# Kernel optimization log

Measured on AMD Instinct MI355X. Metric: run time of the kernel, lower is better.

## Reference

```python
import jax, jax.numpy as jnp
import numpy as np

N, B, E, H, L, NF = 32768, 2048, 524288, 128, 7, 10
NODE_F = 60  # 10 frames * (loc 3 + vel 3)
OUT_F = 30   # 10 frames * 3


def _mlp(x, W1, b1, W2, b2):
    return jax.nn.relu(x @ W1 + b1) @ W2 + b2


def _lin(key, fan_in, fan_out):
    s = 1.0 / np.sqrt(fan_in)
    kw, kb = jax.random.split(key)
    W = jax.random.uniform(kw, (fan_in, fan_out), jnp.float32, -s, s)
    b = jax.random.uniform(kb, (fan_out,), jnp.float32, -s, s)
    return W, b


def setup_inputs() -> dict:
    key = jax.random.key(0)
    ks = jax.random.split(key, 12)
    p = {}
    p["loc"] = jax.random.normal(ks[0], (N, NF, 3), jnp.float32)
    p["vel"] = jax.random.normal(ks[1], (N, NF, 3), jnp.float32)
    p["y"] = jax.random.normal(ks[2], (N, NF, 3), jnp.float32)
    p["edge_index"] = jax.random.randint(ks[3], (2, E), 0, N, dtype=jnp.int64)
    p["batch_size"] = B
    # embedder: Linear(60,H) -> ReLU -> Linear(H,H)
    p["emb_W1"], p["emb_b1"] = _lin(ks[4], NODE_F, H)
    p["emb_W2"], p["emb_b2"] = _lin(ks[5], H, H)
    # per-layer message net Linear(2H,H)->ReLU->Linear(H,H); update net Linear(2H,H)->ReLU->Linear(H,H)
    mW1, mb1, mW2, mb2, uW1, ub1, uW2, ub2 = [], [], [], [], [], [], [], []
    for i in range(L):
        k = jax.random.fold_in(ks[6], i)
        k1, k2, k3, k4 = jax.random.split(k, 4)
        a, b = _lin(k1, 2 * H, H); mW1.append(a); mb1.append(b)
        a, b = _lin(k2, H, H); mW2.append(a); mb2.append(b)
        a, b = _lin(k3, 2 * H, H); uW1.append(a); ub1.append(b)
        a, b = _lin(k4, H, H); uW2.append(a); ub2.append(b)
    p["msg_W1"] = jnp.stack(mW1); p["msg_b1"] = jnp.stack(mb1)
    p["msg_W2"] = jnp.stack(mW2); p["msg_b2"] = jnp.stack(mb2)
    p["upd_W1"] = jnp.stack(uW1); p["upd_b1"] = jnp.stack(ub1)
    p["upd_W2"] = jnp.stack(uW2); p["upd_b2"] = jnp.stack(ub2)
    # head: Linear(H,H) -> ReLU -> Linear(H,30)
    p["head_W1"], p["head_b1"] = _lin(ks[7], H, H)
    p["head_W2"], p["head_b2"] = _lin(ks[8], H, OUT_F)
    return p


def reference(loc, vel, y, edge_index, batch_size,
              emb_W1, emb_b1, emb_W2, emb_b2,
              msg_W1, msg_b1, msg_W2, msg_b2,
              upd_W1, upd_b1, upd_W2, upd_b2,
              head_W1, head_b1, head_W2, head_b2):
    n = loc.shape[0]
    src, dst = edge_index[0], edge_index[1]  # x_j = x[src], x_i = x[dst] (PyG source_to_target)
    x = jnp.concatenate([loc, vel], axis=-1).reshape(n, -1)  # (N, 60)
    x = _mlp(x, emb_W1, emb_b1, emb_W2, emb_b2)              # (N, H)
    for i in range(L):
        m_in = jnp.concatenate([x[dst], x[src]], axis=-1)    # (E, 2H) cat(x_i, x_j)
        msg = _mlp(m_in, msg_W1[i], msg_b1[i], msg_W2[i], msg_b2[i])  # (E, H)
        agg = jax.ops.segment_sum(msg, dst, num_segments=n)  # scatter-add at targets
        x = _mlp(jnp.concatenate([x, agg], axis=-1), upd_W1[i], upd_b1[i], upd_W2[i], upd_b2[i])
    x = _mlp(x, head_W1, head_b1, head_W2, head_b2)          # (N, 30)
    loc_pred = x.reshape(n, NF, 3) + loc
    d = jnp.sqrt(jnp.sum((loc_pred - y) ** 2, axis=-1))      # (N, NF)
    ade_loss = d.reshape(batch_size, -1, NF).mean(axis=-1).mean(axis=-1)  # (B,)
    fde = jnp.sqrt(jnp.sum((loc_pred[:, -1, :] - y[:, -1, :]) ** 2, axis=-1))  # (N,)
    fde_loss = fde.reshape(batch_size, -1).mean(axis=-1)     # (B,)
    backprop_loss = ade_loss.mean()
    return backprop_loss, ade_loss, fde_loss
```

## Files before the change

### kernel.cpp

```cpp
#include <hip/hip_runtime.h>
#include <hip/hip_bf16.h>
#include <stdint.h>

#define HH 128

typedef __attribute__((ext_vector_type(8))) short short8;
typedef __attribute__((ext_vector_type(4))) float floatx4;

typedef __attribute__((address_space(3))) uint32_t lds_u32_t;
typedef const __attribute__((address_space(1))) uint32_t gbl_u32_t;

__device__ __forceinline__ void gl_lds16(const void* g, void* l) {
  __builtin_amdgcn_global_load_lds((gbl_u32_t*)g, (lds_u32_t*)l, 16, 0, 0);
}

__device__ __forceinline__ float bf2f(short v) {
  union { uint32_t u; float f; } x; x.u = ((uint32_t)(uint16_t)v) << 16; return x.f;
}
__device__ __forceinline__ short f2bf(float f) {
  union { float f; uint32_t u; } x; x.f = f;
  uint32_t r = x.u + 0x7fffu + ((x.u >> 16) & 1u);
  return (short)(r >> 16);
}
__device__ __forceinline__ float rdf(const void* p, int i, int fl) {
  return fl ? bf2f(((const short*)p)[i]) : ((const float*)p)[i];
}


__global__ void detect_zero(const int* __restrict__ eidx, int* iflag, int* dflag,
                            int* __restrict__ counts, float* accp, int* ticket,
                            const uint32_t* __restrict__ loc, int N) {
  int g = blockIdx.x * 256 + threadIdx.x;
  if (g < N) counts[g] = 0;
  if (blockIdx.x == 0) {
    __shared__ int nz, cnt;
    if (threadIdx.x == 0) { nz = 0; cnt = 0; *accp = 0.f; *ticket = 0; }
    __syncthreads();
    int any = 0;
    for (int i = threadIdx.x; i < 1024; i += 256) any |= (eidx[2 * i + 1] != 0);
    if (any) atomicOr(&nz, 1);
    uint32_t u = loc[threadIdx.x];
    int e = (u >> 7) & 0xFF;
    if (e >= 100 && e <= 140) atomicAdd(&cnt, 1);
    __syncthreads();
    if (threadIdx.x == 0) {
      *iflag = (nz == 0) ? 1 : 0;
      *dflag = (cnt >= 192) ? 1 : 0;
    }
  }
}


__global__ void pad_input(const void* __restrict__ loc, const void* __restrict__ vel,
                          short* __restrict__ dst, const int* __restrict__ dflag) {
  int fl = *dflag;
  int idx = blockIdx.x * 256 + threadIdx.x;
  int j = idx & 63, i = idx >> 6;
  short v = 0;
  if (j < 60) {
    int f = j / 6, c = j % 6;
    float x = (c < 3) ? rdf(loc, (i * 10 + f) * 3 + c, fl)
                      : rdf(vel, (i * 10 + f) * 3 + (c - 3), fl);
    v = f2bf(x);
  }
  dst[idx] = v;
}

struct WPrep {
  const void* src[8];
  unsigned long long dstoff[8];
  int L[8], K[8], Nn[8], Kp[8], Np[8];
  int bstart[9];
};

__global__ void prep_w(WPrep a, short* __restrict__ wbase, const int* __restrict__ dflag) {
  int fl = *dflag;
  int b = blockIdx.x;
  int s = 0;
  while (b >= a.bstart[s + 1]) ++s;
  int idx = (b - a.bstart[s]) * 256 + threadIdx.x;
  int Kp = a.Kp[s], Np = a.Np[s], K = a.K[s], Nn = a.Nn[s];
  int tot = a.L[s] * Np * Kp;
  if (idx >= tot) return;
  int k = idx % Kp; int rest = idx / Kp; int n = rest % Np; int l = rest / Np;
  short v = 0;
  if (k < K && n < Nn) v = f2bf(rdf(a.src[s], (l * K + k) * Nn + n, fl));
  wbase[a.dstoff[s] + idx] = v;
}

struct BPrep {
  const void* src[8];
  int n[8];
  int estart[9];
};

__global__ void prep_b(BPrep a, float* __restrict__ bias, const int* __restrict__ dflag) {
  int fl = *dflag;
  int idx = blockIdx.x * 256 + threadIdx.x;
  if (idx >= a.estart[8]) return;
  int s = 0;
  while (idx >= a.estart[s + 1]) ++s;
  int j = idx - a.estart[s];
  bias[idx] = (j < a.n[s]) ? rdf(a.src[s], j, fl) : 0.0f;
}


__global__ void fold_kernel(const short* __restrict__ updW1T, const short* __restrict__ msgW2T,
                            short* __restrict__ updW1Tf, const float* __restrict__ msgB2f,
                            float* __restrict__ b2U) {
  if (blockIdx.x < 896) {
    int idx = blockIdx.x * 256 + threadIdx.x;
    int k = idx & 255; int n = (idx >> 8) & 127; int l = idx >> 15;
    if (k < 128) { updW1Tf[idx] = updW1T[idx]; return; }
    int kk = k - 128;
    const short* w2 = msgW2T + l * 128 * 128;
    const short* u1 = updW1T + l * 128 * 256 + n * 256 + 128;
    float s = 0.f;
    for (int j = 0; j < 128; ++j) s += bf2f(w2[j * 128 + kk]) * bf2f(u1[j]);
    updW1Tf[idx] = f2bf(s);
  } else {
    int idx = (blockIdx.x - 896) * 256 + threadIdx.x;
    if (idx >= 7 * 128) return;
    int n = idx & 127, l = idx >> 7;
    const short* u1 = updW1T + l * 128 * 256 + n * 256 + 128;
    const float* b2 = msgB2f + l * 128;
    float s = 0.f;
    for (int j = 0; j < 128; ++j) s += b2[j] * bf2f(u1[j]);
    b2U[idx] = s;
  }
}


__global__ void hist_kernel(const int* __restrict__ eidx, const int* __restrict__ iflag,
                            int* __restrict__ counts, int E) {
  int e = blockIdx.x * 256 + threadIdx.x;
  if (e >= E) return;
  int fl = *iflag;
  int d = fl ? eidx[2 * (E + e)] : eidx[E + e];
  atomicAdd(&counts[d], 1);
}

__global__ void scan_bsum(const int* __restrict__ counts, int* __restrict__ bsums, int N) {
  int i = blockIdx.x * 256 + threadIdx.x;
  int v = (i < N) ? counts[i] : 0;
#pragma unroll
  for (int off = 1; off < 64; off <<= 1) v += __shfl_xor(v, off);
  __shared__ int ws4[4];
  if ((threadIdx.x & 63) == 0) ws4[threadIdx.x >> 6] = v;
  __syncthreads();
  if (threadIdx.x == 0) bsums[blockIdx.x] = ws4[0] + ws4[1] + ws4[2] + ws4[3];
}

__global__ void scan_final(const int* __restrict__ counts, const int* __restrict__ bsums,
                           int* __restrict__ row_start, int* __restrict__ cursor,
                           float* __restrict__ deg, int N, int E) {
  int t = threadIdx.x;
  __shared__ int shb[2];
  __shared__ int wsum[4];
  int v = (t < 128 && t < (int)blockIdx.x) ? bsums[t] : 0;
#pragma unroll
  for (int off = 1; off < 64; off <<= 1) v += __shfl_xor(v, off);
  if (t == 0) shb[0] = v;
  if (t == 64) shb[1] = v;
  int i = blockIdx.x * 256 + t;
  int c = (i < N) ? counts[i] : 0;
  int lane = t & 63, w = t >> 6;
  int x = c;
#pragma unroll
  for (int off = 1; off < 64; off <<= 1) {
    int u = __shfl_up(x, off);
    if (lane >= off) x += u;
  }
  if (lane == 63) wsum[w] = x;
  __syncthreads();
  int wpre = 0;
#pragma unroll
  for (int k = 0; k < 4; ++k)
    if (k < w) wpre += wsum[k];
  int excl = shb[0] + shb[1] + wpre + x - c;
  if (i < N) {
    row_start[i] = excl;
    cursor[i] = excl;
    deg[i] = (float)c;
  }
  if (i == N - 1) row_start[N] = E;
}

__global__ void scatter_kernel(const int* __restrict__ eidx, const int* __restrict__ iflag,
                               int* __restrict__ cursor, int* __restrict__ ssrc, int E) {
  int e = blockIdx.x * 256 + threadIdx.x;
  if (e >= E) return;
  int fl = *iflag;
  int d = fl ? eidx[2 * (E + e)] : eidx[E + e];
  int sv = fl ? eidx[2 * e] : eidx[e];
  int pos = atomicAdd(&cursor[d], 1);
  ssrc[pos] = sv;
}


__global__ __launch_bounds__(256)
void edge_agg(const uint32_t* __restrict__ Pp, const uint32_t* __restrict__ Qp,
              const int* __restrict__ ssrc, const int* __restrict__ row_start,
              uint32_t* __restrict__ Hagg, int Ntot) {
  int w = threadIdx.x >> 6, lane = threadIdx.x & 63;
  int d = blockIdx.x * 4 + w;
  if (d >= Ntot) return;
  uint32_t pv = Pp[(size_t)d * 64 + lane];
  float px = bf2f((short)(pv & 0xffff));
  float py = bf2f((short)(pv >> 16));
  int s0 = row_start[d], s1 = row_start[d + 1];
  float ax = 0.f, ay = 0.f;
  int e = s0;
  for (; e + 8 <= s1; e += 8) {
    int idx[8]; uint32_t q[8];
#pragma unroll
    for (int u = 0; u < 8; ++u) idx[u] = ssrc[e + u];
#pragma unroll
    for (int u = 0; u < 8; ++u) q[u] = Qp[(size_t)idx[u] * 64 + lane];
#pragma unroll
    for (int u = 0; u < 8; ++u) {
      float hx = px + bf2f((short)(q[u] & 0xffff));
      float hy = py + bf2f((short)(q[u] >> 16));
      ax += hx > 0.f ? hx : 0.f;
      ay += hy > 0.f ? hy : 0.f;
    }
  }
  if (e + 4 <= s1) {
    int idx[4]; uint32_t q[4];
#pragma unroll
    for (int u = 0; u < 4; ++u) idx[u] = ssrc[e + u];
#pragma unroll
    for (int u = 0; u < 4; ++u) q[u] = Qp[(size_t)idx[u] * 64 + lane];
#pragma unroll
    for (int u = 0; u < 4; ++u) {
      float hx = px + bf2f((short)(q[u] & 0xffff));
      float hy = py + bf2f((short)(q[u] >> 16));
      ax += hx > 0.f ? hx : 0.f;
      ay += hy > 0.f ? hy : 0.f;
    }
    e += 4;
  }
  if (e + 2 <= s1) {
    int i0 = ssrc[e], i1 = ssrc[e + 1];
    uint32_t q0 = Qp[(size_t)i0 * 64 + lane];
    uint32_t q1 = Qp[(size_t)i1 * 64 + lane];
    float hx = px + bf2f((short)(q0 & 0xffff)), hy = py + bf2f((short)(q0 >> 16));
    ax += hx > 0.f ? hx : 0.f; ay += hy > 0.f ? hy : 0.f;
    hx = px + bf2f((short)(q1 & 0xffff)); hy = py + bf2f((short)(q1 >> 16));
    ax += hx > 0.f ? hx : 0.f; ay += hy > 0.f ? hy : 0.f;
    e += 2;
  }
  if (e < s1) {
    int i0 = ssrc[e];
    uint32_t q0 = Qp[(size_t)i0 * 64 + lane];
    float hx = px + bf2f((short)(q0 & 0xffff));
    float hy = py + bf2f((short)(q0 >> 16));
    ax += hx > 0.f ? hx : 0.f;
    ay += hy > 0.f ? hy : 0.f;
  }
  uint32_t packed = (uint32_t)(uint16_t)f2bf(ax) | ((uint32_t)(uint16_t)f2bf(ay) << 16);
  Hagg[(size_t)d * 64 + lane] = packed;
}


__device__ __forceinline__ void write_aslots64(char* lds, const floatx4 v[2][4],
                                               int wr, int wc, int quad, int l16) {
#pragma unroll
  for (int mt = 0; mt < 2; ++mt) {
    int g = wr * 2 + mt;
#pragma unroll
    for (int nt = 0; nt < 4; ++nt) {
      int s2 = wc * 2 + (nt >> 1);
      int qc = (nt & 1) * 2 + (l16 >> 3);
      char* base = lds + (size_t)(s2 * 4 + g) * 1024 + 2 * (l16 & 7);
#pragma unroll
      for (int r = 0; r < 4; ++r)
        *(short*)(base + (quad * 4 + r + 16 * qc) * 16) = f2bf(v[mt][nt][r]);
    }
  }
}

template <int NT, int TS>
__device__ __forceinline__ void gemm64(const char* lds, int wr, int wc,
                                       floatx4 acc[2][NT], int lane) {
  const char* ldsB = lds + 16384;
#pragma unroll
  for (int s2 = 0; s2 < 4; ++s2) {
    short8 af[2];
#pragma unroll
    for (int mt = 0; mt < 2; ++mt)
      af[mt] = *(const short8*)(lds + (s2 * 4 + wr * 2 + mt) * 1024 + lane * 16);
    short8 bf[NT];
#pragma unroll
    for (int nt = 0; nt < NT; ++nt)
      bf[nt] = *(const short8*)(ldsB + (s2 * TS + wc * NT + nt) * 1024 + lane * 16);
#pragma unroll
    for (int mt = 0; mt < 2; ++mt)
#pragma unroll
      for (int nt = 0; nt < NT; ++nt)
        acc[mt][nt] = __builtin_amdgcn_mfma_f32_16x16x32_bf16(af[mt], bf[nt], acc[mt][nt], 0, 0, 0);
  }
}


template <int MODE>
__global__ __launch_bounds__(256, 2)
void mlp_fused(const short* __restrict__ Asrc, const short* __restrict__ Asrc2,
               const short* __restrict__ W1T, const float* __restrict__ b1,
               const short* __restrict__ W2T, const float* __restrict__ b2,
               const float* __restrict__ deg, const float* __restrict__ b2Uv,
               const short* __restrict__ pqW1, const float* __restrict__ pqB1,
               const short* __restrict__ pq2W, const float* __restrict__ pq2B,
               short* __restrict__ xout, short* __restrict__ Pout,
               short* __restrict__ Qout, float* __restrict__ out32) {
  constexpr int NSA = (MODE == 0) ? 2 : 8;
  constexpr int PQS = (MODE == 3) ? 128 : 256;

  __shared__ __align__(16) char lds[65536];
  char* ldsB = lds + 16384;

  const int tid = threadIdx.x;
  const int w = tid >> 6, lane = tid & 63;
  const int quad = lane >> 4, l16 = lane & 15;
  const int wr = w >> 1, wc = w & 1;
  const int R0 = blockIdx.x * 64;
  const int CB = wc * 64;

  if constexpr (MODE == 0) {
#pragma unroll
    for (int c = 0; c < 4; ++c) {
      int slot = w * 4 + c;
      int s = slot >> 3, t = slot & 7;
      gl_lds16(W1T + (t * 16 + l16) * 64 + s * 32 + quad * 8,
               ldsB + slot * 1024 + lane * 16);
    }
  } else {
#pragma unroll
    for (int c = 0; c < 16; ++c) {
      int slot = w * 16 + c;
      int s = slot >> 3, t = slot & 7;
      gl_lds16(W1T + (t * 16 + l16) * 256 + s * 32 + quad * 8,
               lds + slot * 1024 + lane * 16);
    }
  }

  short8 afrag[NSA][2];
  if constexpr (MODE == 0) {
#pragma unroll
    for (int mt = 0; mt < 2; ++mt) {
      int m = R0 + wr * 32 + mt * 16 + l16;
      const short* pr = Asrc + (size_t)m * 64;
#pragma unroll
      for (int s = 0; s < 2; ++s) afrag[s][mt] = *(const short8*)(pr + s * 32 + quad * 8);
    }
  } else {
#pragma unroll
    for (int mt = 0; mt < 2; ++mt) {
      int m = R0 + wr * 32 + mt * 16 + l16;
      const short* pr = Asrc + (size_t)m * HH;
      const short* ar = Asrc2 + (size_t)m * HH;
#pragma unroll
      for (int s = 0; s < 4; ++s) {
        afrag[s][mt] = *(const short8*)(pr + s * 32 + quad * 8);
        afrag[s + 4][mt] = *(const short8*)(ar + s * 32 + quad * 8);
      }
    }
  }

  float b1f[4], b2f[4], pb1[4], b2u[4];
  float dvals[2][4];
#pragma unroll
  for (int t = 0; t < 4; ++t) {
    int col = CB + t * 16 + l16;
    b1f[t] = b1[col];
    b2f[t] = b2[col];
    pb1[t] = pqB1[col];
  }
  if constexpr (MODE != 0) {
#pragma unroll
    for (int t = 0; t < 4; ++t) b2u[t] = b2Uv[CB + t * 16 + l16];
#pragma unroll
    for (int mt = 0; mt < 2; ++mt)
#pragma unroll
      for (int r = 0; r < 4; ++r)
        dvals[mt][r] = deg[R0 + wr * 32 + mt * 16 + quad * 4 + r];
  }

  __syncthreads();

  floatx4 zero4 = {0.f, 0.f, 0.f, 0.f};
  floatx4 acc[2][4];
#pragma unroll
  for (int mt = 0; mt < 2; ++mt)
#pragma unroll
    for (int t = 0; t < 4; ++t) acc[mt][t] = zero4;
  if constexpr (MODE == 0) {
#pragma unroll
    for (int s = 0; s < 2; ++s) {
      short8 bfrag[4];
#pragma unroll
      for (int nt = 0; nt < 4; ++nt)
        bfrag[nt] = *(const short8*)(ldsB + (s * 8 + wc * 4 + nt) * 1024 + lane * 16);
#pragma unroll
      for (int mt = 0; mt < 2; ++mt)
#pragma unroll
        for (int nt = 0; nt < 4; ++nt)
          acc[mt][nt] = __builtin_amdgcn_mfma_f32_16x16x32_bf16(afrag[s][mt], bfrag[nt], acc[mt][nt], 0, 0, 0);
    }
  } else {
#pragma unroll
    for (int s = 0; s < 8; ++s) {
      short8 bfrag[4];
#pragma unroll
      for (int nt = 0; nt < 4; ++nt)
        bfrag[nt] = *(const short8*)(lds + (s * 8 + wc * 4 + nt) * 1024 + lane * 16);
#pragma unroll
      for (int mt = 0; mt < 2; ++mt)
#pragma unroll
        for (int nt = 0; nt < 4; ++nt)
          acc[mt][nt] = __builtin_amdgcn_mfma_f32_16x16x32_bf16(afrag[s][mt], bfrag[nt], acc[mt][nt], 0, 0, 0);
    }
  }

  __syncthreads();

#pragma unroll
  for (int c = 0; c < 8; ++c) {
    int slot = w * 8 + c;
    int s2 = slot >> 3, t = slot & 7;
    gl_lds16(W2T + (t * 16 + l16) * HH + s2 * 32 + quad * 8,
             ldsB + slot * 1024 + lane * 16);
  }
  {
    floatx4 hv[2][4];
#pragma unroll
    for (int mt = 0; mt < 2; ++mt)
#pragma unroll
      for (int nt = 0; nt < 4; ++nt)
#pragma unroll
        for (int r = 0; r < 4; ++r) {
          float h = acc[mt][nt][r] + b1f[nt];
          if constexpr (MODE != 0) h += dvals[mt][r] * b2u[nt];
          hv[mt][nt][r] = h > 0.f ? h : 0.f;
        }
    write_aslots64(lds, hv, wr, wc, quad, l16);
  }

  __syncthreads();

  floatx4 acc2[2][4];
#pragma unroll
  for (int mt = 0; mt < 2; ++mt)
#pragma unroll
    for (int t = 0; t < 4; ++t) acc2[mt][t] = zero4;
  gemm64<4, 8>(lds, wr, wc, acc2, lane);

  floatx4 xv[2][4];
#pragma unroll
  for (int mt = 0; mt < 2; ++mt)
#pragma unroll
    for (int nt = 0; nt < 4; ++nt)
#pragma unroll
      for (int r = 0; r < 4; ++r)
        xv[mt][nt][r] = acc2[mt][nt][r] + b2f[nt];

  if constexpr (MODE != 3) {
#pragma unroll
    for (int mt = 0; mt < 2; ++mt)
#pragma unroll
      for (int nt = 0; nt < 4; ++nt) {
        int col = CB + nt * 16 + l16;
#pragma unroll
        for (int r = 0; r < 4; ++r) {
          int row = R0 + wr * 32 + mt * 16 + quad * 4 + r;
          xout[(size_t)row * HH + col] = f2bf(xv[mt][nt][r]);
        }
      }
  }

  __syncthreads();

  write_aslots64(lds, xv, wr, wc, quad, l16);
#pragma unroll
  for (int c = 0; c < 8; ++c) {
    int slot = w * 8 + c;
    int s2 = slot >> 3, t = slot & 7;
    gl_lds16(pqW1 + (t * 16 + l16) * PQS + s2 * 32 + quad * 8,
             ldsB + slot * 1024 + lane * 16);
  }

  __syncthreads();

  floatx4 accc[2][4];
#pragma unroll
  for (int mt = 0; mt < 2; ++mt)
#pragma unroll
    for (int t = 0; t < 4; ++t) accc[mt][t] = zero4;
  gemm64<4, 8>(lds, wr, wc, accc, lane);

  if constexpr (MODE == 3) {
    floatx4 h2[2][4];
#pragma unroll
    for (int mt = 0; mt < 2; ++mt)
#pragma unroll
      for (int nt = 0; nt < 4; ++nt)
#pragma unroll
        for (int r = 0; r < 4; ++r) {
          float h = accc[mt][nt][r] + pb1[nt];
          h2[mt][nt][r] = h > 0.f ? h : 0.f;
        }
    __syncthreads();
    write_aslots64(lds, h2, wr, wc, quad, l16);
#pragma unroll
    for (int c = 0; c < 2; ++c) {
      int slot = w * 2 + c;
      int s2 = slot >> 1, t = slot & 1;
      gl_lds16(pq2W + (t * 16 + l16) * 128 + s2 * 32 + quad * 8,
               ldsB + slot * 1024 + lane * 16);
    }
    __syncthreads();
    floatx4 acco[2][1];
#pragma unroll
    for (int mt = 0; mt < 2; ++mt) acco[mt][0] = zero4;
    gemm64<1, 2>(lds, wr, wc, acco, lane);
    float ob = pq2B[wc * 16 + l16];
#pragma unroll
    for (int mt = 0; mt < 2; ++mt) {
      int col = wc * 16 + l16;
#pragma unroll
      for (int r = 0; r < 4; ++r) {
        int row = R0 + wr * 32 + mt * 16 + quad * 4 + r;
        out32[(size_t)row * 32 + col] = acco[mt][0][r] + ob;
      }
    }
  } else {
#pragma unroll
    for (int mt = 0; mt < 2; ++mt)
#pragma unroll
      for (int nt = 0; nt < 4; ++nt) {
        int col = CB + nt * 16 + l16;
#pragma unroll
        for (int r = 0; r < 4; ++r) {
          int row = R0 + wr * 32 + mt * 16 + quad * 4 + r;
          Pout[(size_t)row * HH + col] = f2bf(accc[mt][nt][r] + pb1[nt]);
        }
      }
    __syncthreads();
#pragma unroll
    for (int c = 0; c < 8; ++c) {
      int slot = w * 8 + c;
      int s2 = slot >> 3, t = slot & 7;
      gl_lds16(pqW1 + (t * 16 + l16) * 256 + 128 + s2 * 32 + quad * 8,
               ldsB + slot * 1024 + lane * 16);
    }
    __syncthreads();
    floatx4 accq[2][4];
#pragma unroll
    for (int mt = 0; mt < 2; ++mt)
#pragma unroll
      for (int t = 0; t < 4; ++t) accq[mt][t] = zero4;
    gemm64<4, 8>(lds, wr, wc, accq, lane);
#pragma unroll
    for (int mt = 0; mt < 2; ++mt)
#pragma unroll
      for (int nt = 0; nt < 4; ++nt) {
        int col = CB + nt * 16 + l16;
#pragma unroll
        for (int r = 0; r < 4; ++r) {
          int row = R0 + wr * 32 + mt * 16 + quad * 4 + r;
          Qout[(size_t)row * HH + col] = f2bf(accq[mt][nt][r]);
        }
      }
  }
}


__global__ void loss_kernel(const float* __restrict__ out32, const void* __restrict__ loc,
                            const void* __restrict__ yv, const int* __restrict__ dflag,
                            float* __restrict__ out, float* __restrict__ acc,
                            int* __restrict__ ticket, int NB, int nblocks, float inv) {
  int fl = *dflag;
  int i = blockIdx.x * 256 + threadIdx.x;
  const float* o = out32 + (size_t)i * 32;
  float dsum = 0.f, fde = 0.f;
#pragma unroll
  for (int f = 0; f < 10; ++f) {
    float dx = o[f * 3 + 0] + rdf(loc, i * 30 + f * 3 + 0, fl) - rdf(yv, i * 30 + f * 3 + 0, fl);
    float dy = o[f * 3 + 1] + rdf(loc, i * 30 + f * 3 + 1, fl) - rdf(yv, i * 30 + f * 3 + 1, fl);
    float dz = o[f * 3 + 2] + rdf(loc, i * 30 + f * 3 + 2, fl) - rdf(yv, i * 30 + f * 3 + 2, fl);
    float d = sqrtf(dx * dx + dy * dy + dz * dz);
    dsum += d;
    if (f == 9) fde = d;
  }
#pragma unroll
  for (int m = 1; m < 16; m <<= 1) {
    dsum += __shfl_xor(dsum, m);
    fde += __shfl_xor(fde, m);
  }
  if ((threadIdx.x & 15) == 0) {
    int b = i >> 4;
    out[1 + b] = dsum / 160.0f;
    out[1 + NB + b] = fde / 16.0f;
    unsafeAtomicAdd(acc, dsum);
  }
  __threadfence();
  __syncthreads();
  if (threadIdx.x == 0) {
    int old = atomicAdd(ticket, 1);
    if (old == nblocks - 1) {
      float v = unsafeAtomicAdd(acc, 0.0f);
      out[0] = v * inv;
    }
  }
}


extern "C" void kernel_launch(void* const* d_in, const int* in_sizes, int n_in,
                              void* d_out, int out_size, void* d_ws, size_t ws_size,
                              hipStream_t stream) {
  const void* loc = d_in[0];
  const void* vel = d_in[1];
  const void* yv = d_in[2];
  const int* eidx = (const int*)d_in[3];

  const int N = in_sizes[0] / 30;
  const int E = in_sizes[3] / 2;
  const int L = 7;
  const int NB = N / 16;

  const size_t MB = 1024 * 1024;
  char* ws = (char*)d_ws;
  short* x = (short*)ws;
  short* P = (short*)(ws + 8 * MB);
  short* Qs = (short*)(ws + 24 * MB);
  short* Hagg = (short*)(ws + 32 * MB);
  short* updW1Tf = (short*)(ws + 40 * MB);
  int* bsums = (int*)(ws + 41 * MB);
  short* wbase = (short*)(ws + 48 * MB);
  const unsigned long long OFF_EMBW1 = 0;
  const unsigned long long OFF_EMBW2 = 8192;
  const unsigned long long OFF_HEADW1 = 24576;
  const unsigned long long OFF_HEADW2 = 40960;
  const unsigned long long OFF_MSGW1 = 45056;
  const unsigned long long OFF_MSGW2 = 274432;
  const unsigned long long OFF_UPDW1 = 389120;
  const unsigned long long OFF_UPDW2 = 618496;
  short* embW1T = wbase + OFF_EMBW1;
  short* embW2T = wbase + OFF_EMBW2;
  short* headW1T = wbase + OFF_HEADW1;
  short* headW2T = wbase + OFF_HEADW2;
  short* msgW1T = wbase + OFF_MSGW1;
  short* msgW2T = wbase + OFF_MSGW2;
  short* updW1T = wbase + OFF_UPDW1;
  short* updW2T = wbase + OFF_UPDW2;
  float* bias = (float*)(ws + 49 * MB + 512 * 1024);
  float* embB1f = bias;
  float* embB2f = bias + 128;
  float* msgB1f = bias + 256;
  float* msgB2f = bias + 1152;
  float* updB1f = bias + 2048;
  float* updB2f = bias + 2944;
  float* headB1f = bias + 3840;
  float* headB2f = bias + 3968;
  float* b2U = bias + 4096;
  int* counts = (int*)(ws + 49 * MB + 768 * 1024);
  int* row_start = (int*)(ws + 50 * MB);
  int* cursor = (int*)(ws + 50 * MB + 256 * 1024);
  float* deg = (float*)(ws + 50 * MB + 512 * 1024);
  int* iflag = (int*)(ws + 50 * MB + 768 * 1024);
  int* dflag = iflag + 16;
  float* accp = (float*)(iflag + 32);
  int* ticket = iflag + 48;
  int* ssrc = (int*)(ws + 51 * MB);
  short* in64 = (short*)(ws + 53 * MB);
  float* out32 = (float*)(ws + 57 * MB);

  const int NBLK = (N + 255) / 256;

  detect_zero<<<NBLK, 256, 0, stream>>>(eidx, iflag, dflag, counts, accp, ticket,
                                        (const uint32_t*)loc, N);
  hist_kernel<<<(E + 255) / 256, 256, 0, stream>>>(eidx, iflag, counts, E);
  scan_bsum<<<NBLK, 256, 0, stream>>>(counts, bsums, N);
  scan_final<<<NBLK, 256, 0, stream>>>(counts, bsums, row_start, cursor, deg, N, E);
  scatter_kernel<<<(E + 255) / 256, 256, 0, stream>>>(eidx, iflag, cursor, ssrc, E);

  pad_input<<<(N * 64) / 256, 256, 0, stream>>>(loc, vel, in64, dflag);

  {
    WPrep a;
    const void* srcs[8] = {d_in[5], d_in[7], d_in[17], d_in[19],
                           d_in[9], d_in[11], d_in[13], d_in[15]};
    unsigned long long offs[8] = {OFF_EMBW1, OFF_EMBW2, OFF_HEADW1, OFF_HEADW2,
                                  OFF_MSGW1, OFF_MSGW2, OFF_UPDW1, OFF_UPDW2};
    int Ls[8] = {1, 1, 1, 1, 7, 7, 7, 7};
    int Ks[8] = {60, 128, 128, 128, 256, 128, 256, 128};
    int Ns[8] = {128, 128, 128, 30, 128, 128, 128, 128};
    int Kps[8] = {64, 128, 128, 128, 256, 128, 256, 128};
    int Nps[8] = {128, 128, 128, 32, 128, 128, 128, 128};
    int cum = 0;
    for (int s = 0; s < 8; ++s) {
      a.src[s] = srcs[s]; a.dstoff[s] = offs[s];
      a.L[s] = Ls[s]; a.K[s] = Ks[s]; a.Nn[s] = Ns[s]; a.Kp[s] = Kps[s]; a.Np[s] = Nps[s];
      a.bstart[s] = cum;
      cum += (Ls[s] * Nps[s] * Kps[s] + 255) / 256;
    }
    a.bstart[8] = cum;
    prep_w<<<cum, 256, 0, stream>>>(a, wbase, dflag);
  }
  {
    BPrep a;
    const void* srcs[8] = {d_in[6], d_in[8], d_in[10], d_in[12],
                           d_in[14], d_in[16], d_in[18], d_in[20]};
    int ns[8] = {128, 128, 896, 896, 896, 896, 128, 30};
    int es[9] = {0, 128, 256, 1152, 2048, 2944, 3840, 3968, 4000};
    for (int s = 0; s < 8; ++s) { a.src[s] = srcs[s]; a.n[s] = ns[s]; a.estart[s] = es[s]; }
    a.estart[8] = es[8];
    prep_b<<<16, 256, 0, stream>>>(a, bias, dflag);
  }

  fold_kernel<<<900, 256, 0, stream>>>(updW1T, msgW2T, updW1Tf, msgB2f, b2U);

  mlp_fused<0><<<N / 64, 256, 0, stream>>>(in64, nullptr,
      embW1T, embB1f, embW2T, embB2f, nullptr, nullptr,
      msgW1T, msgB1f, nullptr, nullptr, x, P, Qs, nullptr);

  for (int l = 0; l < L; ++l) {
    edge_agg<<<(N + 3) / 4, 256, 0, stream>>>((const uint32_t*)P, (const uint32_t*)Qs,
                                              ssrc, row_start, (uint32_t*)Hagg, N);
    if (l < L - 1) {
      mlp_fused<2><<<N / 64, 256, 0, stream>>>(x, Hagg,
          updW1Tf + l * 128 * 256, updB1f + l * 128, updW2T + l * 128 * 128, updB2f + l * 128,
          deg, b2U + l * 128,
          msgW1T + (l + 1) * 128 * 256, msgB1f + (l + 1) * 128, nullptr, nullptr,
          x, P, Qs, nullptr);
    } else {
      mlp_fused<3><<<N / 64, 256, 0, stream>>>(x, Hagg,
          updW1Tf + l * 128 * 256, updB1f + l * 128, updW2T + l * 128 * 128, updB2f + l * 128,
          deg, b2U + l * 128,
          headW1T, headB1f, headW2T, headB2f,
          nullptr, nullptr, nullptr, out32);
    }
  }

  loss_kernel<<<N / 256, 256, 0, stream>>>(out32, loc, yv, dflag, (float*)d_out, accp,
                                           ticket, NB, N / 256, 1.0f / 327680.0f);
}
```

Baseline: 508.2 us.

## Fold update second linear into next-layer weights to skip x materialization

Precomputes products of each update net's W2 with the following message-W1 halves, update-W1 x-half and head W1, plus their folded biases, in an extended fold kernel. Each layer kernel then takes the precomputed XU term from the previous layer as an additive input, so it runs only 128-wide K GEMMs and never materializes x. The first-layer GEMM shrinks from K=256 to K=128, LDS use drops to 48KB and the occupancy hint rises to 3 blocks per CU. It adds an extra XU output GEMM per layer and more bf16 rounding from the folded matrices.

```diff
diff --git a/kernel.cpp b/kernel.cpp
--- a/kernel.cpp
+++ b/kernel.cpp
@@ -105,28 +105,68 @@
 }
 
 
-__global__ void fold_kernel(const short* __restrict__ updW1T, const short* __restrict__ msgW2T,
-                            short* __restrict__ updW1Tf, const float* __restrict__ msgB2f,
-                            float* __restrict__ b2U) {
-  if (blockIdx.x < 896) {
+__global__ void fold_kernel(const short* __restrict__ msgW1T, const short* __restrict__ msgW2T,
+                            const short* __restrict__ updW1T, const short* __restrict__ updW2T,
+                            const short* __restrict__ headW1T,
+                            const float* __restrict__ msgB1f, const float* __restrict__ msgB2f,
+                            const float* __restrict__ updB1f, const float* __restrict__ updB2f,
+                            const float* __restrict__ headB1f,
+                            short* __restrict__ fmats, float* __restrict__ fbias) {
+  if (blockIdx.x < 1664) {
     int idx = blockIdx.x * 256 + threadIdx.x;
-    int k = idx & 255; int n = (idx >> 8) & 127; int l = idx >> 15;
-    if (k < 128) { updW1Tf[idx] = updW1T[idx]; return; }
-    int kk = k - 128;
-    const short* w2 = msgW2T + l * 128 * 128;
-    const short* u1 = updW1T + l * 128 * 256 + n * 256 + 128;
+    if (idx >= 26 * 16384) return;
+    int k = idx & 127; int n = (idx >> 7) & 127; int m = idx >> 14;
+    const short* w2;
+    const short* rhs;
+    if (m < 7) {
+      w2 = msgW2T + m * 16384;
+      rhs = updW1T + m * 32768 + n * 256 + 128;
+    } else if (m < 14) {
+      int l = m - 7;
+      w2 = updW2T + l * 16384;
+      rhs = (l < 6) ? (msgW1T + (l + 1) * 32768 + n * 256) : (headW1T + n * 128);
+    } else if (m < 20) {
+      int l = m - 14;
+      w2 = updW2T + l * 16384;
+      rhs = msgW1T + (l + 1) * 32768 + n * 256 + 128;
+    } else {
+      int l = m - 20;
+      w2 = updW2T + l * 16384;
+      rhs = updW1T + (l + 1) * 32768 + n * 256;
+    }
     float s = 0.f;
-    for (int j = 0; j < 128; ++j) s += bf2f(w2[j * 128 + kk]) * bf2f(u1[j]);
-    updW1Tf[idx] = f2bf(s);
+    for (int j = 0; j < 128; ++j) s += bf2f(w2[j * 128 + k]) * bf2f(rhs[j]);
+    fmats[idx] = f2bf(s);
   } else {
-    int idx = (blockIdx.x - 896) * 256 + threadIdx.x;
-    if (idx >= 7 * 128) return;
-    int n = idx & 127, l = idx >> 7;
-    const short* u1 = updW1T + l * 128 * 256 + n * 256 + 128;
-    const float* b2 = msgB2f + l * 128;
+    int idx = (blockIdx.x - 1664) * 256 + threadIdx.x;
+    if (idx >= 26 * 128) return;
+    int n = idx & 127; int m = idx >> 7;
     float s = 0.f;
-    for (int j = 0; j < 128; ++j) s += b2[j] * bf2f(u1[j]);
-    b2U[idx] = s;
+    if (m < 7) {
+      const short* u1 = updW1T + m * 32768 + n * 256 + 128;
+      for (int j = 0; j < 128; ++j) s += msgB2f[m * 128 + j] * bf2f(u1[j]);
+    } else if (m < 14) {
+      int l = m - 7;
+      if (l < 6) {
+        const short* m1 = msgW1T + (l + 1) * 32768 + n * 256;
+        for (int j = 0; j < 128; ++j) s += updB2f[l * 128 + j] * bf2f(m1[j]);
+        s += msgB1f[(l + 1) * 128 + n];
+      } else {
+        const short* h1 = headW1T + n * 128;
+        for (int j = 0; j < 128; ++j) s += updB2f[6 * 128 + j] * bf2f(h1[j]);
+        s += headB1f[n];
+      }
+    } else if (m < 20) {
+      int l = m - 14;
+      const short* m1 = msgW1T + (l + 1) * 32768 + n * 256 + 128;
+      for (int j = 0; j < 128; ++j) s += updB2f[l * 128 + j] * bf2f(m1[j]);
+    } else {
+      int l = m - 20;
+      const short* u1 = updW1T + (l + 1) * 32768 + n * 256;
+      for (int j = 0; j < 128; ++j) s += updB2f[l * 128 + j] * bf2f(u1[j]);
+      s += updB1f[(l + 1) * 128 + n];
+    }
+    fbias[m * 128 + n] = s;
   }
 }
 
@@ -302,21 +342,28 @@
   }
 }
 
+__device__ __forceinline__ void stage128(const short* M, int stride, char* ldsB,
+                                         int w, int lane, int quad, int l16) {
+#pragma unroll
+  for (int c = 0; c < 8; ++c) {
+    int slot = w * 8 + c, s2 = slot >> 3, t = slot & 7;
+    gl_lds16(M + (t * 16 + l16) * stride + s2 * 32 + quad * 8,
+             ldsB + slot * 1024 + lane * 16);
+  }
+}
+
 
 template <int MODE>
-__global__ __launch_bounds__(256, 2)
-void mlp_fused(const short* __restrict__ Asrc, const short* __restrict__ Asrc2,
-               const short* __restrict__ W1T, const float* __restrict__ b1,
-               const short* __restrict__ W2T, const float* __restrict__ b2,
-               const float* __restrict__ deg, const float* __restrict__ b2Uv,
-               const short* __restrict__ pqW1, const float* __restrict__ pqB1,
-               const short* __restrict__ pq2W, const float* __restrict__ pq2B,
-               short* __restrict__ xout, short* __restrict__ Pout,
-               short* __restrict__ Qout, float* __restrict__ out32) {
-  constexpr int NSA = (MODE == 0) ? 2 : 8;
-  constexpr int PQS = (MODE == 3) ? 128 : 256;
-
-  __shared__ __align__(16) char lds[65536];
+__global__ __launch_bounds__(256, 3)
+void mlp_fused(const short* __restrict__ Ain, const short* __restrict__ XUin,
+               const short* __restrict__ W1s, const float* __restrict__ b1s,
+               const short* __restrict__ W2s, const float* __restrict__ b2s,
+               const short* __restrict__ W3s, const float* __restrict__ b3s,
+               const short* __restrict__ W4s, const float* __restrict__ b4s,
+               const float* __restrict__ deg,
+               short* __restrict__ Pout, short* __restrict__ Qout,
+               short* __restrict__ XUout, float* __restrict__ out32) {
+  __shared__ __align__(16) char lds[49152];
   char* ldsB = lds + 16384;
 
   const int tid = threadIdx.x;
@@ -326,77 +373,177 @@
   const int R0 = blockIdx.x * 64;
   const int CB = wc * 64;
 
+  floatx4 zero4 = {0.f, 0.f, 0.f, 0.f};
+  floatx4 acc[2][4];
+
   if constexpr (MODE == 0) {
 #pragma unroll
     for (int c = 0; c < 4; ++c) {
-      int slot = w * 4 + c;
-      int s = slot >> 3, t = slot & 7;
-      gl_lds16(W1T + (t * 16 + l16) * 64 + s * 32 + quad * 8,
+      int slot = w * 4 + c, s = slot >> 3, t = slot & 7;
+      gl_lds16(W1s + (t * 16 + l16) * 64 + s * 32 + quad * 8,
                ldsB + slot * 1024 + lane * 16);
     }
-  } else {
-#pragma unroll
-    for (int c = 0; c < 16; ++c) {
-      int slot = w * 16 + c;
-      int s = slot >> 3, t = slot & 7;
-      gl_lds16(W1T + (t * 16 + l16) * 256 + s * 32 + quad * 8,
-               lds + slot * 1024 + lane * 16);
-    }
-  }
-
-  short8 afrag[NSA][2];
-  if constexpr (MODE == 0) {
+    short8 afrag[2][2];
 #pragma unroll
     for (int mt = 0; mt < 2; ++mt) {
       int m = R0 + wr * 32 + mt * 16 + l16;
-      const short* pr = Asrc + (size_t)m * 64;
+      const short* pr = Ain + (size_t)m * 64;
 #pragma unroll
       for (int s = 0; s < 2; ++s) afrag[s][mt] = *(const short8*)(pr + s * 32 + quad * 8);
     }
+    float b1f[4], b2f[4], pa[4], pc[4];
+#pragma unroll
+    for (int t = 0; t < 4; ++t) {
+      int col = CB + t * 16 + l16;
+      b1f[t] = b1s[col]; b2f[t] = b2s[col]; pa[t] = b3s[col]; pc[t] = b4s[col];
+    }
+#pragma unroll
+    for (int mt = 0; mt < 2; ++mt)
+#pragma unroll
+      for (int t = 0; t < 4; ++t) acc[mt][t] = zero4;
+    __syncthreads();
+#pragma unroll
+    for (int s = 0; s < 2; ++s) {
+      short8 bfrag[4];
+#pragma unroll
+      for (int nt = 0; nt < 4; ++nt)
+        bfrag[nt] = *(const short8*)(ldsB + (s * 8 + wc * 4 + nt) * 1024 + lane * 16);
+#pragma unroll
+      for (int mt = 0; mt < 2; ++mt)
+#pragma unroll
+        for (int nt = 0; nt < 4; ++nt)
+          acc[mt][nt] = __builtin_amdgcn_mfma_f32_16x16x32_bf16(afrag[s][mt], bfrag[nt], acc[mt][nt], 0, 0, 0);
+    }
+    __syncthreads();
+    stage128(W2s, 128, ldsB, w, lane, quad, l16);
+    {
+      floatx4 hv[2][4];
+#pragma unroll
+      for (int mt = 0; mt < 2; ++mt)
+#pragma unroll
+        for (int nt = 0; nt < 4; ++nt)
+#pragma unroll
+          for (int r = 0; r < 4; ++r) {
+            float h = acc[mt][nt][r] + b1f[nt];
+            hv[mt][nt][r] = h > 0.f ? h : 0.f;
+          }
+      write_aslots64(lds, hv, wr, wc, quad, l16);
+    }
+    __syncthreads();
+    floatx4 accx[2][4];
+#pragma unroll
+    for (int mt = 0; mt < 2; ++mt)
+#pragma unroll
+      for (int t = 0; t < 4; ++t) accx[mt][t] = zero4;
+    gemm64<4, 8>(lds, wr, wc, accx, lane);
+    floatx4 xv[2][4];
+#pragma unroll
+    for (int mt = 0; mt < 2; ++mt)
+#pragma unroll
+      for (int nt = 0; nt < 4; ++nt)
+#pragma unroll
+        for (int r = 0; r < 4; ++r)
+          xv[mt][nt][r] = accx[mt][nt][r] + b2f[nt];
+    __syncthreads();
+    write_aslots64(lds, xv, wr, wc, quad, l16);
+    stage128(W3s, 256, ldsB, w, lane, quad, l16);
+    __syncthreads();
+    floatx4 ap[2][4];
+#pragma unroll
+    for (int mt = 0; mt < 2; ++mt)
+#pragma unroll
+      for (int t = 0; t < 4; ++t) ap[mt][t] = zero4;
+    gemm64<4, 8>(lds, wr, wc, ap, lane);
+#pragma unroll
+    for (int mt = 0; mt < 2; ++mt)
+#pragma unroll
+      for (int nt = 0; nt < 4; ++nt) {
+        int col = CB + nt * 16 + l16;
+#pragma unroll
+        for (int r = 0; r < 4; ++r) {
+          int row = R0 + wr * 32 + mt * 16 + quad * 4 + r;
+          Pout[(size_t)row * HH + col] = f2bf(ap[mt][nt][r] + pa[nt]);
+        }
+      }
+    __syncthreads();
+    stage128(W3s + 128, 256, ldsB, w, lane, quad, l16);
+    __syncthreads();
+    floatx4 aq[2][4];
+#pragma unroll
+    for (int mt = 0; mt < 2; ++mt)
+#pragma unroll
+      for (int t = 0; t < 4; ++t) aq[mt][t] = zero4;
+    gemm64<4, 8>(lds, wr, wc, aq, lane);
+#pragma unroll
+    for (int mt = 0; mt < 2; ++mt)
+#pragma unroll
+      for (int nt = 0; nt < 4; ++nt) {
+        int col = CB + nt * 16 + l16;
+#pragma unroll
+        for (int r = 0; r < 4; ++r) {
+          int row = R0 + wr * 32 + mt * 16 + quad * 4 + r;
+          Qout[(size_t)row * HH + col] = f2bf(aq[mt][nt][r]);
+        }
+      }
+    __syncthreads();
+    stage128(W4s, 256, ldsB, w, lane, quad, l16);
+    __syncthreads();
+    floatx4 au[2][4];
+#pragma unroll
+    for (int mt = 0; mt < 2; ++mt)
+#pragma unroll
+      for (int t = 0; t < 4; ++t) au[mt][t] = zero4;
+    gemm64<4, 8>(lds, wr, wc, au, lane);
+#pragma unroll
+    for (int mt = 0; mt < 2; ++mt)
+#pragma unroll
+      for (int nt = 0; nt < 4; ++nt) {
+        int col = CB + nt * 16 + l16;
+#pragma unroll
+        for (int r = 0; r < 4; ++r) {
+          int row = R0 + wr * 32 + mt * 16 + quad * 4 + r;
+          XUout[(size_t)row * HH + col] = f2bf(au[mt][nt][r] + pc[nt]);
+        }
+      }
+    return;
   } else {
+    stage128(W1s, 128, ldsB, w, lane, quad, l16);
+    short8 hfrag[4][2];
 #pragma unroll
     for (int mt = 0; mt < 2; ++mt) {
       int m = R0 + wr * 32 + mt * 16 + l16;
-      const short* pr = Asrc + (size_t)m * HH;
-      const short* ar = Asrc2 + (size_t)m * HH;
-#pragma unroll
-      for (int s = 0; s < 4; ++s) {
-        afrag[s][mt] = *(const short8*)(pr + s * 32 + quad * 8);
-        afrag[s + 4][mt] = *(const short8*)(ar + s * 32 + quad * 8);
-      }
-    }
-  }
-
-  float b1f[4], b2f[4], pb1[4], b2u[4];
-  float dvals[2][4];
-#pragma unroll
-  for (int t = 0; t < 4; ++t) {
-    int col = CB + t * 16 + l16;
-    b1f[t] = b1[col];
-    b2f[t] = b2[col];
-    pb1[t] = pqB1[col];
-  }
-  if constexpr (MODE != 0) {
-#pragma unroll
-    for (int t = 0; t < 4; ++t) b2u[t] = b2Uv[CB + t * 16 + l16];
+      const short* pr = Ain + (size_t)m * HH;
+#pragma unroll
+      for (int s = 0; s < 4; ++s) hfrag[s][mt] = *(const short8*)(pr + s * 32 + quad * 8);
+    }
+    float b2u[4], pa[4], pb[4], pc[4];
+#pragma unroll
+    for (int t = 0; t < 4; ++t) {
+      int col = CB + t * 16 + l16;
+      b2u[t] = b1s[col];
+      pa[t] = b2s[col];
+      if constexpr (MODE == 2) { pb[t] = b3s[col]; pc[t] = b4s[col]; }
+    }
+    float dvals[2][4];
 #pragma unroll
     for (int mt = 0; mt < 2; ++mt)
 #pragma unroll
       for (int r = 0; r < 4; ++r)
         dvals[mt][r] = deg[R0 + wr * 32 + mt * 16 + quad * 4 + r];
-  }
-
-  __syncthreads();
-
-  floatx4 zero4 = {0.f, 0.f, 0.f, 0.f};
-  floatx4 acc[2][4];
-#pragma unroll
-  for (int mt = 0; mt < 2; ++mt)
-#pragma unroll
-    for (int t = 0; t < 4; ++t) acc[mt][t] = zero4;
-  if constexpr (MODE == 0) {
-#pragma unroll
-    for (int s = 0; s < 2; ++s) {
+#pragma unroll
+    for (int mt = 0; mt < 2; ++mt)
+#pragma unroll
+      for (int nt = 0; nt < 4; ++nt) {
+        int col = CB + nt * 16 + l16;
+#pragma unroll
+        for (int r = 0; r < 4; ++r) {
+          int row = R0 + wr * 32 + mt * 16 + quad * 4 + r;
+          acc[mt][nt][r] = bf2f(XUin[(size_t)row * HH + col]) + dvals[mt][r] * b2u[nt];
+        }
+      }
+    __syncthreads();
+#pragma unroll
+    for (int s = 0; s < 4; ++s) {
       short8 bfrag[4];
 #pragma unroll
       for (int nt = 0; nt < 4; ++nt)
@@ -405,172 +552,118 @@
       for (int mt = 0; mt < 2; ++mt)
 #pragma unroll
         for (int nt = 0; nt < 4; ++nt)
-          acc[mt][nt] = __builtin_amdgcn_mfma_f32_16x16x32_bf16(afrag[s][mt], bfrag[nt], acc[mt][nt], 0, 0, 0);
-    }
-  } else {
-#pragma unroll
-    for (int s = 0; s < 8; ++s) {
-      short8 bfrag[4];
-#pragma unroll
-      for (int nt = 0; nt < 4; ++nt)
-        bfrag[nt] = *(const short8*)(lds + (s * 8 + wc * 4 + nt) * 1024 + lane * 16);
+          acc[mt][nt] = __builtin_amdgcn_mfma_f32_16x16x32_bf16(hfrag[s][mt], bfrag[nt], acc[mt][nt], 0, 0, 0);
+    }
+    __syncthreads();
+    stage128(W2s, 128, ldsB, w, lane, quad, l16);
+    {
+      floatx4 hv[2][4];
 #pragma unroll
       for (int mt = 0; mt < 2; ++mt)
 #pragma unroll
         for (int nt = 0; nt < 4; ++nt)
-          acc[mt][nt] = __builtin_amdgcn_mfma_f32_16x16x32_bf16(afrag[s][mt], bfrag[nt], acc[mt][nt], 0, 0, 0);
-    }
-  }
-
-  __syncthreads();
-
-#pragma unroll
-  for (int c = 0; c < 8; ++c) {
-    int slot = w * 8 + c;
-    int s2 = slot >> 3, t = slot & 7;
-    gl_lds16(W2T + (t * 16 + l16) * HH + s2 * 32 + quad * 8,
-             ldsB + slot * 1024 + lane * 16);
-  }
-  {
-    floatx4 hv[2][4];
-#pragma unroll
-    for (int mt = 0; mt < 2; ++mt)
-#pragma unroll
-      for (int nt = 0; nt < 4; ++nt)
-#pragma unroll
-        for (int r = 0; r < 4; ++r) {
-          float h = acc[mt][nt][r] + b1f[nt];
-          if constexpr (MODE != 0) h += dvals[mt][r] * b2u[nt];
-          hv[mt][nt][r] = h > 0.f ? h : 0.f;
+#pragma unroll
+          for (int r = 0; r < 4; ++r) {
+            float h = acc[mt][nt][r];
+            hv[mt][nt][r] = h > 0.f ? h : 0.f;
+          }
+      write_aslots64(lds, hv, wr, wc, quad, l16);
+    }
+    __syncthreads();
+    floatx4 ap[2][4];
+#pragma unroll
+    for (int mt = 0; mt < 2; ++mt)
+#pragma unroll
+      for (int t = 0; t < 4; ++t) ap[mt][t] = zero4;
+    gemm64<4, 8>(lds, wr, wc, ap, lane);
+
+    if constexpr (MODE == 2) {
+#pragma unroll
+      for (int mt = 0; mt < 2; ++mt)
+#pragma unroll
+        for (int nt = 0; nt < 4; ++nt) {
+          int col = CB + nt * 16 + l16;
+#pragma unroll
+          for (int r = 0; r < 4; ++r) {
+            int row = R0 + wr * 32 + mt * 16 + quad * 4 + r;
+            Pout[(size_t)row * HH + col] = f2bf(ap[mt][nt][r] + pa[nt]);
+          }
         }
-    write_aslots64(lds, hv, wr, wc, quad, l16);
-  }
-
-  __syncthreads();
-
-  floatx4 acc2[2][4];
-#pragma unroll
-  for (int mt = 0; mt < 2; ++mt)
-#pragma unroll
-    for (int t = 0; t < 4; ++t) acc2[mt][t] = zero4;
-  gemm64<4, 8>(lds, wr, wc, acc2, lane);
-
-  floatx4 xv[2][4];
-#pragma unroll
-  for (int mt = 0; mt < 2; ++mt)
-#pragma unroll
-    for (int nt = 0; nt < 4; ++nt)
-#pragma unroll
-      for (int r = 0; r < 4; ++r)
-        xv[mt][nt][r] = acc2[mt][nt][r] + b2f[nt];
-
-  if constexpr (MODE != 3) {
-#pragma unroll
-    for (int mt = 0; mt < 2; ++mt)
-#pragma unroll
-      for (int nt = 0; nt < 4; ++nt) {
-        int col = CB + nt * 16 + l16;
+      __syncthreads();
+      stage128(W3s, 128, ldsB, w, lane, quad, l16);
+      __syncthreads();
+      floatx4 aq[2][4];
+#pragma unroll
+      for (int mt = 0; mt < 2; ++mt)
+#pragma unroll
+        for (int t = 0; t < 4; ++t) aq[mt][t] = zero4;
+      gemm64<4, 8>(lds, wr, wc, aq, lane);
+#pragma unroll
+      for (int mt = 0; mt < 2; ++mt)
+#pragma unroll
+        for (int nt = 0; nt < 4; ++nt) {
+          int col = CB + nt * 16 + l16;
+#pragma unroll
+          for (int r = 0; r < 4; ++r) {
+            int row = R0 + wr * 32 + mt * 16 + quad * 4 + r;
+            Qout[(size_t)row * HH + col] = f2bf(aq[mt][nt][r] + pb[nt]);
+          }
+        }
+      __syncthreads();
+      stage128(W4s, 128, ldsB, w, lane, quad, l16);
+      __syncthreads();
+      floatx4 au[2][4];
+#pragma unroll
+      for (int mt = 0; mt < 2; ++mt)
+#pragma unroll
+        for (int t = 0; t < 4; ++t) au[mt][t] = zero4;
+      gemm64<4, 8>(lds, wr, wc, au, lane);
+#pragma unroll
+      for (int mt = 0; mt < 2; ++mt)
+#pragma unroll
+        for (int nt = 0; nt < 4; ++nt) {
+          int col = CB + nt * 16 + l16;
+#pragma unroll
+          for (int r = 0; r < 4; ++r) {
+            int row = R0 + wr * 32 + mt * 16 + quad * 4 + r;
+            XUout[(size_t)row * HH + col] = f2bf(au[mt][nt][r] + pc[nt]);
+          }
+        }
+    } else {
+      floatx4 h2[2][4];
+#pragma unroll
+      for (int mt = 0; mt < 2; ++mt)
+#pragma unroll
+        for (int nt = 0; nt < 4; ++nt)
+#pragma unroll
+          for (int r = 0; r < 4; ++r) {
+            float h = ap[mt][nt][r] + pa[nt];
+            h2[mt][nt][r] = h > 0.f ? h : 0.f;
+          }
+      __syncthreads();
+      write_aslots64(lds, h2, wr, wc, quad, l16);
+#pragma unroll
+      for (int c = 0; c < 2; ++c) {
+        int slot = w * 2 + c, s2 = slot >> 1, t = slot & 1;
+        gl_lds16(W3s + (t * 16 + l16) * 128 + s2 * 32 + quad * 8,
+                 ldsB + slot * 1024 + lane * 16);
+      }
+      __syncthreads();
+      floatx4 acco[2][1];
+#pragma unroll
+      for (int mt = 0; mt < 2; ++mt) acco[mt][0] = zero4;
+      gemm64<1, 2>(lds, wr, wc, acco, lane);
+      float ob = b3s[wc * 16 + l16];
+#pragma unroll
+      for (int mt = 0; mt < 2; ++mt) {
+        int col = wc * 16 + l16;
 #pragma unroll
         for (int r = 0; r < 4; ++r) {
           int row = R0 + wr * 32 + mt * 16 + quad * 4 + r;
-          xout[(size_t)row * HH + col] = f2bf(xv[mt][nt][r]);
+          out32[(size_t)row * 32 + col] = acco[mt][0][r] + ob;
         }
       }
-  }
-
-  __syncthreads();
-
-  write_aslots64(lds, xv, wr, wc, quad, l16);
-#pragma unroll
-  for (int c = 0; c < 8; ++c) {
-    int slot = w * 8 + c;
-    int s2 = slot >> 3, t = slot & 7;
-    gl_lds16(pqW1 + (t * 16 + l16) * PQS + s2 * 32 + quad * 8,
-             ldsB + slot * 1024 + lane * 16);
-  }
-
-  __syncthreads();
-
-  floatx4 accc[2][4];
-#pragma unroll
-  for (int mt = 0; mt < 2; ++mt)
-#pragma unroll
-    for (int t = 0; t < 4; ++t) accc[mt][t] = zero4;
-  gemm64<4, 8>(lds, wr, wc, accc, lane);
-
-  if constexpr (MODE == 3) {
-    floatx4 h2[2][4];
-#pragma unroll
-    for (int mt = 0; mt < 2; ++mt)
-#pragma unroll
-      for (int nt = 0; nt < 4; ++nt)
-#pragma unroll
-        for (int r = 0; r < 4; ++r) {
-          float h = accc[mt][nt][r] + pb1[nt];
-          h2[mt][nt][r] = h > 0.f ? h : 0.f;
-        }
-    __syncthreads();
-    write_aslots64(lds, h2, wr, wc, quad, l16);
-#pragma unroll
-    for (int c = 0; c < 2; ++c) {
-      int slot = w * 2 + c;
-      int s2 = slot >> 1, t = slot & 1;
-      gl_lds16(pq2W + (t * 16 + l16) * 128 + s2 * 32 + quad * 8,
-               ldsB + slot * 1024 + lane * 16);
-    }
-    __syncthreads();
-    floatx4 acco[2][1];
-#pragma unroll
-    for (int mt = 0; mt < 2; ++mt) acco[mt][0] = zero4;
-    gemm64<1, 2>(lds, wr, wc, acco, lane);
-    float ob = pq2B[wc * 16 + l16];
-#pragma unroll
-    for (int mt = 0; mt < 2; ++mt) {
-      int col = wc * 16 + l16;
-#pragma unroll
-      for (int r = 0; r < 4; ++r) {
-        int row = R0 + wr * 32 + mt * 16 + quad * 4 + r;
-        out32[(size_t)row * 32 + col] = acco[mt][0][r] + ob;
-      }
-    }
-  } else {
-#pragma unroll
-    for (int mt = 0; mt < 2; ++mt)
-#pragma unroll
-      for (int nt = 0; nt < 4; ++nt) {
-        int col = CB + nt * 16 + l16;
-#pragma unroll
-        for (int r = 0; r < 4; ++r) {
-          int row = R0 + wr * 32 + mt * 16 + quad * 4 + r;
-          Pout[(size_t)row * HH + col] = f2bf(accc[mt][nt][r] + pb1[nt]);
-        }
-      }
-    __syncthreads();
-#pragma unroll
-    for (int c = 0; c < 8; ++c) {
-      int slot = w * 8 + c;
-      int s2 = slot >> 3, t = slot & 7;
-      gl_lds16(pqW1 + (t * 16 + l16) * 256 + 128 + s2 * 32 + quad * 8,
-               ldsB + slot * 1024 + lane * 16);
-    }
-    __syncthreads();
-    floatx4 accq[2][4];
-#pragma unroll
-    for (int mt = 0; mt < 2; ++mt)
-#pragma unroll
-      for (int t = 0; t < 4; ++t) accq[mt][t] = zero4;
-    gemm64<4, 8>(lds, wr, wc, accq, lane);
-#pragma unroll
-    for (int mt = 0; mt < 2; ++mt)
-#pragma unroll
-      for (int nt = 0; nt < 4; ++nt) {
-        int col = CB + nt * 16 + l16;
-#pragma unroll
-        for (int r = 0; r < 4; ++r) {
-          int row = R0 + wr * 32 + mt * 16 + quad * 4 + r;
-          Qout[(size_t)row * HH + col] = f2bf(accq[mt][nt][r]);
-        }
-      }
+    }
   }
 }
 
@@ -630,11 +723,11 @@
 
   const size_t MB = 1024 * 1024;
   char* ws = (char*)d_ws;
-  short* x = (short*)ws;
+  short* XU = (short*)ws;
   short* P = (short*)(ws + 8 * MB);
   short* Qs = (short*)(ws + 24 * MB);
   short* Hagg = (short*)(ws + 32 * MB);
-  short* updW1Tf = (short*)(ws + 40 * MB);
+  short* fmats = (short*)(ws + 40 * MB);
   int* bsums = (int*)(ws + 41 * MB);
   short* wbase = (short*)(ws + 48 * MB);
   const unsigned long long OFF_EMBW1 = 0;
@@ -662,7 +755,7 @@
   float* updB2f = bias + 2944;
   float* headB1f = bias + 3840;
   float* headB2f = bias + 3968;
-  float* b2U = bias + 4096;
+  float* fbias = (float*)(ws + 49 * MB + 640 * 1024);
   int* counts = (int*)(ws + 49 * MB + 768 * 1024);
   int* row_start = (int*)(ws + 50 * MB);
   int* cursor = (int*)(ws + 50 * MB + 256 * 1024);
@@ -718,27 +811,32 @@
     prep_b<<<16, 256, 0, stream>>>(a, bias, dflag);
   }
 
-  fold_kernel<<<900, 256, 0, stream>>>(updW1T, msgW2T, updW1Tf, msgB2f, b2U);
+  fold_kernel<<<1664 + 13, 256, 0, stream>>>(msgW1T, msgW2T, updW1T, updW2T, headW1T,
+                                             msgB1f, msgB2f, updB1f, updB2f, headB1f,
+                                             fmats, fbias);
 
   mlp_fused<0><<<N / 64, 256, 0, stream>>>(in64, nullptr,
-      embW1T, embB1f, embW2T, embB2f, nullptr, nullptr,
-      msgW1T, msgB1f, nullptr, nullptr, x, P, Qs, nullptr);
+      embW1T, embB1f, embW2T, embB2f,
+      msgW1T, msgB1f, updW1T, updB1f,
+      nullptr, P, Qs, XU, nullptr);
 
   for (int l = 0; l < L; ++l) {
     edge_agg<<<(N + 3) / 4, 256, 0, stream>>>((const uint32_t*)P, (const uint32_t*)Qs,
                                               ssrc, row_start, (uint32_t*)Hagg, N);
     if (l < L - 1) {
-      mlp_fused<2><<<N / 64, 256, 0, stream>>>(x, Hagg,
-          updW1Tf + l * 128 * 256, updB1f + l * 128, updW2T + l * 128 * 128, updB2f + l * 128,
-          deg, b2U + l * 128,
-          msgW1T + (l + 1) * 128 * 256, msgB1f + (l + 1) * 128, nullptr, nullptr,
-          x, P, Qs, nullptr);
+      mlp_fused<2><<<N / 64, 256, 0, stream>>>(Hagg, XU,
+          fmats + l * 16384, fbias + l * 128,
+          fmats + (7 + l) * 16384, fbias + (7 + l) * 128,
+          fmats + (14 + l) * 16384, fbias + (14 + l) * 128,
+          fmats + (20 + l) * 16384, fbias + (20 + l) * 128,
+          deg, P, Qs, XU, nullptr);
     } else {
-      mlp_fused<3><<<N / 64, 256, 0, stream>>>(x, Hagg,
-          updW1Tf + l * 128 * 256, updB1f + l * 128, updW2T + l * 128 * 128, updB2f + l * 128,
-          deg, b2U + l * 128,
-          headW1T, headB1f, headW2T, headB2f,
-          nullptr, nullptr, nullptr, out32);
+      mlp_fused<3><<<N / 64, 256, 0, stream>>>(Hagg, XU,
+          fmats + 6 * 16384, fbias + 6 * 128,
+          fmats + 13 * 16384, fbias + 13 * 128,
+          headW2T, headB2f,
+          nullptr, nullptr,
+          deg, nullptr, nullptr, nullptr, out32);
     }
   }
 
```

Measured after the change: 485.9 us. 4.4% less time.
